# Kernel tuning notes

Measured on AMD Instinct MI355X. Metric: run time of the kernel, lower is better.

## Reference

```python
import math
import jax, jax.numpy as jnp
import numpy as np

NUM_HEADS = 16

def setup_inputs() -> dict:
    key = jax.random.key(0)
    ks = jax.random.split(key, 6)
    B, S, d = 16, 1024, 1024
    scale = 1.0 / math.sqrt(d)
    x = jax.random.normal(ks[0], (B, S, d), dtype=jnp.float32)
    Wq = jax.random.normal(ks[1], (d, d), dtype=jnp.float32) * scale
    Wk = jax.random.normal(ks[2], (d, d), dtype=jnp.float32) * scale
    Wv = jax.random.normal(ks[3], (d, d), dtype=jnp.float32) * scale
    Wo = jax.random.normal(ks[4], (d, d), dtype=jnp.float32) * scale
    z = jnp.zeros((d,), dtype=jnp.float32)
    return {"x": x, "Wq": Wq, "bq": z, "Wk": Wk, "bk": z, "Wv": Wv, "bv": z, "Wo": Wo, "bo": z}

def _split_heads(t, H):
    B, S, d = t.shape
    return t.reshape(B, S, H, d // H).transpose(0, 2, 1, 3)  # [B,H,S,dh]

def reference(x, Wq, bq, Wk, bk, Wv, bv, Wo, bo):
    B, S, d = x.shape
    H = NUM_HEADS
    dh = d // H
    # torch Linear: x @ W.T + b
    Q = _split_heads(x @ Wq.T + bq, H)
    K = _split_heads(x @ Wk.T + bk, H)
    V = _split_heads(x @ Wv.T + bv, H)
    scores = jnp.einsum('bhqd,bhkd->bhqk', Q, K)  # [B,H,S,S]
    causal = jnp.arange(S)[None, :] <= jnp.arange(S)[:, None]  # [S,S] True = allowed
    mask = (1.0 - causal.astype(jnp.float32)) * -100000.0
    # NOTE: original divides (scores + mask) by sqrt(dh), mask included
    attn = jax.nn.softmax((scores + mask) / math.sqrt(dh), axis=-1)
    out = jnp.einsum('bhqk,bhkd->bhqd', attn, V)  # [B,H,S,dh]
    out = out.transpose(0, 2, 1, 3).reshape(B, S, d)
    return out @ Wo.T + bo
```

## Files before the change

### kernel.cpp

```cpp
#include <hip/hip_runtime.h>

#define B_  16
#define S_  1024
#define D_  1024
#define H_  16
#define DH_ 64
#define M_  (B_ * S_)
#define BH_ (B_ * H_)

typedef __attribute__((ext_vector_type(8))) __bf16 bf16x8;
typedef __attribute__((ext_vector_type(4))) float  f32x4;

__device__ __forceinline__ ushort f2bf(float f) {
  unsigned u = __builtin_bit_cast(unsigned, f);
  return (ushort)((u + 0x7FFFu + ((u >> 16) & 1u)) >> 16);
}

__device__ __forceinline__ bf16x8 ld8(const ushort* p) {
  return *(const bf16x8*)p;
}

__device__ __forceinline__ float fast_exp2(float x) {
  return __builtin_amdgcn_exp2f(x);
}

__device__ __forceinline__ void gl_lds16(const void* g, void* s) {
  __builtin_amdgcn_global_load_lds((__attribute__((address_space(1))) void*)g,
                                   (__attribute__((address_space(3))) void*)s,
                                   16, 0, 0);
}

__global__ void cvt4(const float* __restrict__ s, ushort* __restrict__ d, int n4) {
  int i = blockIdx.x * 256 + threadIdx.x;
  if (i < n4) {
    const float4 v = ((const float4*)s)[i];
    ushort4 o;
    o.x = f2bf(v.x); o.y = f2bf(v.y); o.z = f2bf(v.z); o.w = f2bf(v.w);
    ((ushort4*)d)[i] = o;
  }
}

template <int MODE>
__global__ void gemm_bt(const ushort* __restrict__ A, const ushort* __restrict__ W,
                        const float* __restrict__ bias, ushort* __restrict__ outH,
                        float* __restrict__ outF, int M, int N, int K) {
  __shared__ ushort lA[128 * 32];
  __shared__ ushort lB[128 * 32];
  const int w  = threadIdx.x >> 6;
  const int l  = threadIdx.x & 63;
  const int m0 = blockIdx.y * 128, n0 = blockIdx.x * 128;
  const int srow = (w << 4) + (l >> 2);
  const int scol = (l & 3) << 3;
  const int lr = l & 15, qd = l >> 4;
  const int wm = (w >> 1) << 6, wn = (w & 1) << 6;

  const f32x4 z = {0.f, 0.f, 0.f, 0.f};
  f32x4 acc[4][4];
#pragma unroll
  for (int i = 0; i < 4; i++)
#pragma unroll
    for (int j = 0; j < 4; j++) acc[i][j] = z;

  for (int k0 = 0; k0 < K; k0 += 32) {
#pragma unroll
    for (int r = 0; r < 2; r++) {
      const int row = r * 64 + srow;
      gl_lds16(A + (size_t)(m0 + row) * K + k0 + scol, &lA[row * 32 + scol]);
      gl_lds16(W + (size_t)(n0 + row) * K + k0 + scol, &lB[row * 32 + scol]);
    }
    __syncthreads();
    bf16x8 af[4], bf_[4];
#pragma unroll
    for (int t = 0; t < 4; t++) {
      af[t]  = ld8(&lA[(wm + t * 16 + lr) * 32 + qd * 8]);
      bf_[t] = ld8(&lB[(wn + t * 16 + lr) * 32 + qd * 8]);
    }
#pragma unroll
    for (int i = 0; i < 4; i++)
#pragma unroll
      for (int j = 0; j < 4; j++)
        acc[i][j] = __builtin_amdgcn_mfma_f32_16x16x32_bf16(af[i], bf_[j], acc[i][j], 0, 0, 0);
    __syncthreads();
  }

#pragma unroll
  for (int j = 0; j < 4; j++) {
    const int n = n0 + wn + j * 16 + lr;
    const float bv = bias[n];
#pragma unroll
    for (int i = 0; i < 4; i++) {
      const f32x4 v = acc[i][j];
#pragma unroll
      for (int r = 0; r < 4; r++) {
        const int m = m0 + wm + i * 16 + qd * 4 + r;
        const float val = v[r] + bv;
        if (MODE == 2) {
          outF[(size_t)m * N + n] = val;
        } else {
          const int b = m >> 10, s = m & 1023, h = n >> 6, dc = n & 63;
          if (MODE == 0)
            outH[((size_t)(b * H_ + h) * S_ + s) * DH_ + dc] = f2bf(val);
          else
            outH[((size_t)(b * H_ + h) * DH_ + dc) * S_ + s] = f2bf(val);
        }
      }
    }
  }
}

#define PSTR 40
__global__ __launch_bounds__(256) void attn_kernel(
    const ushort* __restrict__ Q, const ushort* __restrict__ K,
    const ushort* __restrict__ Vt, ushort* __restrict__ O) {
  __shared__ ushort lP[4][64 * PSTR];
  const int bh = blockIdx.y;
  const int w = threadIdx.x >> 6, l = threadIdx.x & 63;
  const int lr = l & 15, qd = l >> 4;
  const int q0 = (blockIdx.x * 4 + w) * 64;
  const size_t base = (size_t)bh * (S_ * DH_);
  const ushort* Qb = Q + base;
  const ushort* Kb = K + base;
  const ushort* Vb = Vt + (size_t)bh * (DH_ * S_);
  ushort* myP = &lP[w][0];

  bf16x8 bq[4][2];
#pragma unroll
  for (int qt = 0; qt < 4; qt++)
#pragma unroll
    for (int kc = 0; kc < 2; kc++)
      bq[qt][kc] = ld8(Qb + (size_t)(q0 + qt * 16 + lr) * DH_ + kc * 32 + qd * 8);

  const f32x4 z = {0.f, 0.f, 0.f, 0.f};
  f32x4 acc[4][4];
#pragma unroll
  for (int i = 0; i < 4; i++)
#pragma unroll
    for (int j = 0; j < 4; j++) acc[i][j] = z;
  float li[4] = {0.f, 0.f, 0.f, 0.f};

  const float C = 0.18033688011112042f;

  for (int kb = 0; kb < q0 + 64; kb += 32) {
    bf16x8 ak[2][2];
#pragma unroll
    for (int kt = 0; kt < 2; kt++)
#pragma unroll
      for (int kc = 0; kc < 2; kc++)
        ak[kt][kc] = ld8(Kb + (size_t)(kb + kt * 16 + lr) * DH_ + kc * 32 + qd * 8);
    bf16x8 av[4];
#pragma unroll
    for (int dt = 0; dt < 4; dt++)
      av[dt] = ld8(Vb + (size_t)(dt * 16 + lr) * S_ + kb + qd * 8);

    const bool diag = (kb + 31 >= q0);
#pragma unroll
    for (int kt = 0; kt < 2; kt++) {
      const int keyb = kb + kt * 16 + qd * 4;
#pragma unroll
      for (int qt = 0; qt < 4; qt++) {
        f32x4 s = z;
        s = __builtin_amdgcn_mfma_f32_16x16x32_bf16(ak[kt][0], bq[qt][0], s, 0, 0, 0);
        s = __builtin_amdgcn_mfma_f32_16x16x32_bf16(ak[kt][1], bq[qt][1], s, 0, 0, 0);
        const int qq = q0 + qt * 16 + lr;
        float e0 = s[0] * C, e1 = s[1] * C, e2 = s[2] * C, e3 = s[3] * C;
        if (diag) {
          e0 = (keyb + 0 <= qq) ? e0 : -1e30f;
          e1 = (keyb + 1 <= qq) ? e1 : -1e30f;
          e2 = (keyb + 2 <= qq) ? e2 : -1e30f;
          e3 = (keyb + 3 <= qq) ? e3 : -1e30f;
        }
        const float p0 = fast_exp2(e0), p1 = fast_exp2(e1);
        const float p2 = fast_exp2(e2), p3 = fast_exp2(e3);
        li[qt] += (p0 + p1) + (p2 + p3);
        const uint d0 = __builtin_amdgcn_perm(__builtin_bit_cast(uint, p1),
                                              __builtin_bit_cast(uint, p0), 0x07060302u);
        const uint d1 = __builtin_amdgcn_perm(__builtin_bit_cast(uint, p3),
                                              __builtin_bit_cast(uint, p2), 0x07060302u);
        uint2 pk; pk.x = d0; pk.y = d1;
        *(uint2*)(myP + (qt * 16 + lr) * PSTR + kt * 16 + qd * 4) = pk;
      }
    }
#pragma unroll
    for (int qt = 0; qt < 4; qt++) {
      const bf16x8 bp = ld8(myP + (qt * 16 + lr) * PSTR + qd * 8);
#pragma unroll
      for (int dt = 0; dt < 4; dt++)
        acc[dt][qt] = __builtin_amdgcn_mfma_f32_16x16x32_bf16(av[dt], bp, acc[dt][qt], 0, 0, 0);
    }
  }

  const int b = bh >> 4, h = bh & 15;
#pragma unroll
  for (int qt = 0; qt < 4; qt++) {
    float s = li[qt];
    s += __shfl_xor(s, 16);
    s += __shfl_xor(s, 32);
    const float inv = 1.f / s;
    const int q = q0 + qt * 16 + lr;
    ushort* orow = O + ((size_t)(b * S_ + q) * D_) + h * DH_ + qd * 4;
#pragma unroll
    for (int dt = 0; dt < 4; dt++) {
      const f32x4 v = acc[dt][qt];
      uint2 pk;
      pk.x = (uint)f2bf(v[0] * inv) | ((uint)f2bf(v[1] * inv) << 16);
      pk.y = (uint)f2bf(v[2] * inv) | ((uint)f2bf(v[3] * inv) << 16);
      *(uint2*)(orow + dt * 16) = pk;
    }
  }
}

extern "C" void kernel_launch(void* const* d_in, const int* in_sizes, int n_in,
                              void* d_out, int out_size, void* d_ws, size_t ws_size,
                              hipStream_t stream) {
  const float* x  = (const float*)d_in[0];
  const float* Wq = (const float*)d_in[1];
  const float* bq = (const float*)d_in[2];
  const float* Wk = (const float*)d_in[3];
  const float* bk = (const float*)d_in[4];
  const float* Wv = (const float*)d_in[5];
  const float* bv = (const float*)d_in[6];
  const float* Wo = (const float*)d_in[7];
  const float* bo = (const float*)d_in[8];
  float* out = (float*)d_out;

  char* ws = (char*)d_ws;
  ushort* xb   = (ushort*)(ws);
  ushort* qb   = (ushort*)(ws + 33554432);
  ushort* kb   = (ushort*)(ws + 67108864);
  ushort* vtb  = (ushort*)(ws + 100663296);
  ushort* attn = (ushort*)(ws + 134217728);
  ushort* wqb  = (ushort*)(ws + 167772160);
  ushort* wkb  = (ushort*)(ws + 169869312);
  ushort* wvb  = (ushort*)(ws + 171966464);
  ushort* wob  = (ushort*)(ws + 174063616);

  cvt4<<<16384, 256, 0, stream>>>(x,  xb,  4194304);
  cvt4<<<1024,  256, 0, stream>>>(Wq, wqb, 262144);
  cvt4<<<1024,  256, 0, stream>>>(Wk, wkb, 262144);
  cvt4<<<1024,  256, 0, stream>>>(Wv, wvb, 262144);
  cvt4<<<1024,  256, 0, stream>>>(Wo, wob, 262144);

  dim3 g(D_ / 128, M_ / 128);
  gemm_bt<0><<<g, 256, 0, stream>>>(xb, wqb, bq, qb,  nullptr, M_, D_, D_);
  gemm_bt<0><<<g, 256, 0, stream>>>(xb, wkb, bk, kb,  nullptr, M_, D_, D_);
  gemm_bt<1><<<g, 256, 0, stream>>>(xb, wvb, bv, vtb, nullptr, M_, D_, D_);

  attn_kernel<<<dim3(4, BH_), 256, 0, stream>>>(qb, kb, vtb, attn);

  gemm_bt<2><<<g, 256, 0, stream>>>(attn, wob, bo, nullptr, out, M_, D_, D_);
}
```

Before: 469.0 us.

## Fuse QKV projections into one GEMM and balance causal attention work per wave

Replaces three separate projection GEMM launches with one launch over a concatenated weight matrix, choosing bias and output layout per column block. The attention kernel now has each wave process a pair of query tiles (p and 15-p), so causal work is equal across waves and blocks, with half as many blocks. Fewer blocks lowers parallelism, and the fused GEMM relies on the converted weights being contiguous in the workspace.

```diff
diff --git a/kernel.cpp b/kernel.cpp
--- a/kernel.cpp
+++ b/kernel.cpp
@@ -40,10 +40,10 @@
   }
 }
 
-template <int MODE>
-__global__ void gemm_bt(const ushort* __restrict__ A, const ushort* __restrict__ W,
-                        const float* __restrict__ bias, ushort* __restrict__ outH,
-                        float* __restrict__ outF, int M, int N, int K) {
+__global__ void gemm_qkv(const ushort* __restrict__ A, const ushort* __restrict__ Wqkv,
+                         const float* __restrict__ bqp, const float* __restrict__ bkp,
+                         const float* __restrict__ bvp, ushort* __restrict__ qO,
+                         ushort* __restrict__ kO, ushort* __restrict__ vtO) {
   __shared__ ushort lA[128 * 32];
   __shared__ ushort lB[128 * 32];
   const int w  = threadIdx.x >> 6;
@@ -53,6 +53,76 @@
   const int scol = (l & 3) << 3;
   const int lr = l & 15, qd = l >> 4;
   const int wm = (w >> 1) << 6, wn = (w & 1) << 6;
+  const int K = D_;
+
+  const f32x4 z = {0.f, 0.f, 0.f, 0.f};
+  f32x4 acc[4][4];
+#pragma unroll
+  for (int i = 0; i < 4; i++)
+#pragma unroll
+    for (int j = 0; j < 4; j++) acc[i][j] = z;
+
+  for (int k0 = 0; k0 < K; k0 += 32) {
+#pragma unroll
+    for (int r = 0; r < 2; r++) {
+      const int row = r * 64 + srow;
+      gl_lds16(A    + (size_t)(m0 + row) * K + k0 + scol, &lA[row * 32 + scol]);
+      gl_lds16(Wqkv + (size_t)(n0 + row) * K + k0 + scol, &lB[row * 32 + scol]);
+    }
+    __syncthreads();
+    bf16x8 af[4], bf_[4];
+#pragma unroll
+    for (int t = 0; t < 4; t++) {
+      af[t]  = ld8(&lA[(wm + t * 16 + lr) * 32 + qd * 8]);
+      bf_[t] = ld8(&lB[(wn + t * 16 + lr) * 32 + qd * 8]);
+    }
+#pragma unroll
+    for (int i = 0; i < 4; i++)
+#pragma unroll
+      for (int j = 0; j < 4; j++)
+        acc[i][j] = __builtin_amdgcn_mfma_f32_16x16x32_bf16(af[i], bf_[j], acc[i][j], 0, 0, 0);
+    __syncthreads();
+  }
+
+  const int proj = n0 >> 10;
+  const float* bias = (proj == 0) ? bqp : (proj == 1) ? bkp : bvp;
+  ushort* outH = (proj == 0) ? qO : (proj == 1) ? kO : vtO;
+  const int nb = n0 & 1023;
+
+#pragma unroll
+  for (int j = 0; j < 4; j++) {
+    const int n = nb + wn + j * 16 + lr;
+    const float bv = bias[n];
+    const int h = n >> 6, dc = n & 63;
+#pragma unroll
+    for (int i = 0; i < 4; i++) {
+      const f32x4 v = acc[i][j];
+#pragma unroll
+      for (int r = 0; r < 4; r++) {
+        const int m = m0 + wm + i * 16 + qd * 4 + r;
+        const int b = m >> 10, s = m & 1023;
+        const float val = v[r] + bv;
+        if (proj < 2)
+          outH[((size_t)(b * H_ + h) * S_ + s) * DH_ + dc] = f2bf(val);
+        else
+          outH[((size_t)(b * H_ + h) * DH_ + dc) * S_ + s] = f2bf(val);
+      }
+    }
+  }
+}
+
+__global__ void gemm_out(const ushort* __restrict__ A, const ushort* __restrict__ W,
+                         const float* __restrict__ bias, float* __restrict__ outF) {
+  __shared__ ushort lA[128 * 32];
+  __shared__ ushort lB[128 * 32];
+  const int w  = threadIdx.x >> 6;
+  const int l  = threadIdx.x & 63;
+  const int m0 = blockIdx.y * 128, n0 = blockIdx.x * 128;
+  const int srow = (w << 4) + (l >> 2);
+  const int scol = (l & 3) << 3;
+  const int lr = l & 15, qd = l >> 4;
+  const int wm = (w >> 1) << 6, wn = (w & 1) << 6;
+  const int K = D_, N = D_;
 
   const f32x4 z = {0.f, 0.f, 0.f, 0.f};
   f32x4 acc[4][4];
@@ -93,16 +163,7 @@
 #pragma unroll
       for (int r = 0; r < 4; r++) {
         const int m = m0 + wm + i * 16 + qd * 4 + r;
-        const float val = v[r] + bv;
-        if (MODE == 2) {
-          outF[(size_t)m * N + n] = val;
-        } else {
-          const int b = m >> 10, s = m & 1023, h = n >> 6, dc = n & 63;
-          if (MODE == 0)
-            outH[((size_t)(b * H_ + h) * S_ + s) * DH_ + dc] = f2bf(val);
-          else
-            outH[((size_t)(b * H_ + h) * DH_ + dc) * S_ + s] = f2bf(val);
-        }
+        outF[(size_t)m * N + n] = v[r] + bv;
       }
     }
   }
@@ -116,95 +177,99 @@
   const int bh = blockIdx.y;
   const int w = threadIdx.x >> 6, l = threadIdx.x & 63;
   const int lr = l & 15, qd = l >> 4;
-  const int q0 = (blockIdx.x * 4 + w) * 64;
+  const int p = blockIdx.x * 4 + w;
   const size_t base = (size_t)bh * (S_ * DH_);
   const ushort* Qb = Q + base;
   const ushort* Kb = K + base;
   const ushort* Vb = Vt + (size_t)bh * (DH_ * S_);
   ushort* myP = &lP[w][0];
-
-  bf16x8 bq[4][2];
-#pragma unroll
-  for (int qt = 0; qt < 4; qt++)
-#pragma unroll
-    for (int kc = 0; kc < 2; kc++)
-      bq[qt][kc] = ld8(Qb + (size_t)(q0 + qt * 16 + lr) * DH_ + kc * 32 + qd * 8);
-
+  const int b = bh >> 4, h = bh & 15;
+  const float C = 0.18033688011112042f;
   const f32x4 z = {0.f, 0.f, 0.f, 0.f};
-  f32x4 acc[4][4];
-#pragma unroll
-  for (int i = 0; i < 4; i++)
-#pragma unroll
-    for (int j = 0; j < 4; j++) acc[i][j] = z;
-  float li[4] = {0.f, 0.f, 0.f, 0.f};
-
-  const float C = 0.18033688011112042f;
-
-  for (int kb = 0; kb < q0 + 64; kb += 32) {
-    bf16x8 ak[2][2];
-#pragma unroll
-    for (int kt = 0; kt < 2; kt++)
+
+#pragma unroll 1
+  for (int tt = 0; tt < 2; tt++) {
+    const int q0 = (tt == 0 ? p : 15 - p) * 64;
+
+    bf16x8 bq[4][2];
+#pragma unroll
+    for (int qt = 0; qt < 4; qt++)
 #pragma unroll
       for (int kc = 0; kc < 2; kc++)
-        ak[kt][kc] = ld8(Kb + (size_t)(kb + kt * 16 + lr) * DH_ + kc * 32 + qd * 8);
-    bf16x8 av[4];
-#pragma unroll
-    for (int dt = 0; dt < 4; dt++)
-      av[dt] = ld8(Vb + (size_t)(dt * 16 + lr) * S_ + kb + qd * 8);
-
-    const bool diag = (kb + 31 >= q0);
-#pragma unroll
-    for (int kt = 0; kt < 2; kt++) {
-      const int keyb = kb + kt * 16 + qd * 4;
+        bq[qt][kc] = ld8(Qb + (size_t)(q0 + qt * 16 + lr) * DH_ + kc * 32 + qd * 8);
+
+    f32x4 acc[4][4];
+#pragma unroll
+    for (int i = 0; i < 4; i++)
+#pragma unroll
+      for (int j = 0; j < 4; j++) acc[i][j] = z;
+    float li[4] = {0.f, 0.f, 0.f, 0.f};
+
+    for (int kb = 0; kb < q0 + 64; kb += 32) {
+      bf16x8 ak[2][2];
+#pragma unroll
+      for (int kt = 0; kt < 2; kt++)
+#pragma unroll
+        for (int kc = 0; kc < 2; kc++)
+          ak[kt][kc] = ld8(Kb + (size_t)(kb + kt * 16 + lr) * DH_ + kc * 32 + qd * 8);
+      bf16x8 av[4];
+#pragma unroll
+      for (int dt = 0; dt < 4; dt++)
+        av[dt] = ld8(Vb + (size_t)(dt * 16 + lr) * S_ + kb + qd * 8);
+
+      const bool diag = (kb + 31 >= q0);
+#pragma unroll
+      for (int kt = 0; kt < 2; kt++) {
+        const int keyb = kb + kt * 16 + qd * 4;
+#pragma unroll
+        for (int qt = 0; qt < 4; qt++) {
+          f32x4 s = z;
+          s = __builtin_amdgcn_mfma_f32_16x16x32_bf16(ak[kt][0], bq[qt][0], s, 0, 0, 0);
+          s = __builtin_amdgcn_mfma_f32_16x16x32_bf16(ak[kt][1], bq[qt][1], s, 0, 0, 0);
+          const int qq = q0 + qt * 16 + lr;
+          float e0 = s[0] * C, e1 = s[1] * C, e2 = s[2] * C, e3 = s[3] * C;
+          if (diag) {
+            e0 = (keyb + 0 <= qq) ? e0 : -1e30f;
+            e1 = (keyb + 1 <= qq) ? e1 : -1e30f;
+            e2 = (keyb + 2 <= qq) ? e2 : -1e30f;
+            e3 = (keyb + 3 <= qq) ? e3 : -1e30f;
+          }
+          const float p0 = fast_exp2(e0), p1 = fast_exp2(e1);
+          const float p2 = fast_exp2(e2), p3 = fast_exp2(e3);
+          li[qt] += (p0 + p1) + (p2 + p3);
+          const uint d0 = __builtin_amdgcn_perm(__builtin_bit_cast(uint, p1),
+                                                __builtin_bit_cast(uint, p0), 0x07060302u);
+          const uint d1 = __builtin_amdgcn_perm(__builtin_bit_cast(uint, p3),
+                                                __builtin_bit_cast(uint, p2), 0x07060302u);
+          uint2 pk; pk.x = d0; pk.y = d1;
+          *(uint2*)(myP + (qt * 16 + lr) * PSTR + kt * 16 + qd * 4) = pk;
+        }
+      }
 #pragma unroll
       for (int qt = 0; qt < 4; qt++) {
-        f32x4 s = z;
-        s = __builtin_amdgcn_mfma_f32_16x16x32_bf16(ak[kt][0], bq[qt][0], s, 0, 0, 0);
-        s = __builtin_amdgcn_mfma_f32_16x16x32_bf16(ak[kt][1], bq[qt][1], s, 0, 0, 0);
-        const int qq = q0 + qt * 16 + lr;
-        float e0 = s[0] * C, e1 = s[1] * C, e2 = s[2] * C, e3 = s[3] * C;
-        if (diag) {
-          e0 = (keyb + 0 <= qq) ? e0 : -1e30f;
-          e1 = (keyb + 1 <= qq) ? e1 : -1e30f;
-          e2 = (keyb + 2 <= qq) ? e2 : -1e30f;
-          e3 = (keyb + 3 <= qq) ? e3 : -1e30f;
-        }
-        const float p0 = fast_exp2(e0), p1 = fast_exp2(e1);
-        const float p2 = fast_exp2(e2), p3 = fast_exp2(e3);
-        li[qt] += (p0 + p1) + (p2 + p3);
-        const uint d0 = __builtin_amdgcn_perm(__builtin_bit_cast(uint, p1),
-                                              __builtin_bit_cast(uint, p0), 0x07060302u);
-        const uint d1 = __builtin_amdgcn_perm(__builtin_bit_cast(uint, p3),
-                                              __builtin_bit_cast(uint, p2), 0x07060302u);
-        uint2 pk; pk.x = d0; pk.y = d1;
-        *(uint2*)(myP + (qt * 16 + lr) * PSTR + kt * 16 + qd * 4) = pk;
-      }
-    }
+        const bf16x8 bp = ld8(myP + (qt * 16 + lr) * PSTR + qd * 8);
+#pragma unroll
+        for (int dt = 0; dt < 4; dt++)
+          acc[dt][qt] = __builtin_amdgcn_mfma_f32_16x16x32_bf16(av[dt], bp, acc[dt][qt], 0, 0, 0);
+      }
+    }
+
 #pragma unroll
     for (int qt = 0; qt < 4; qt++) {
-      const bf16x8 bp = ld8(myP + (qt * 16 + lr) * PSTR + qd * 8);
-#pragma unroll
-      for (int dt = 0; dt < 4; dt++)
-        acc[dt][qt] = __builtin_amdgcn_mfma_f32_16x16x32_bf16(av[dt], bp, acc[dt][qt], 0, 0, 0);
-    }
-  }
-
-  const int b = bh >> 4, h = bh & 15;
-#pragma unroll
-  for (int qt = 0; qt < 4; qt++) {
-    float s = li[qt];
-    s += __shfl_xor(s, 16);
-    s += __shfl_xor(s, 32);
-    const float inv = 1.f / s;
-    const int q = q0 + qt * 16 + lr;
-    ushort* orow = O + ((size_t)(b * S_ + q) * D_) + h * DH_ + qd * 4;
-#pragma unroll
-    for (int dt = 0; dt < 4; dt++) {
-      const f32x4 v = acc[dt][qt];
-      uint2 pk;
-      pk.x = (uint)f2bf(v[0] * inv) | ((uint)f2bf(v[1] * inv) << 16);
-      pk.y = (uint)f2bf(v[2] * inv) | ((uint)f2bf(v[3] * inv) << 16);
-      *(uint2*)(orow + dt * 16) = pk;
+      float s = li[qt];
+      s += __shfl_xor(s, 16);
+      s += __shfl_xor(s, 32);
+      const float inv = 1.f / s;
+      const int q = q0 + qt * 16 + lr;
+      ushort* orow = O + ((size_t)(b * S_ + q) * D_) + h * DH_ + qd * 4;
+#pragma unroll
+      for (int dt = 0; dt < 4; dt++) {
+        const f32x4 v = acc[dt][qt];
+        uint2 pk;
+        pk.x = (uint)f2bf(v[0] * inv) | ((uint)f2bf(v[1] * inv) << 16);
+        pk.y = (uint)f2bf(v[2] * inv) | ((uint)f2bf(v[3] * inv) << 16);
+        *(uint2*)(orow + dt * 16) = pk;
+      }
     }
   }
 }
@@ -240,12 +305,9 @@
   cvt4<<<1024,  256, 0, stream>>>(Wv, wvb, 262144);
   cvt4<<<1024,  256, 0, stream>>>(Wo, wob, 262144);
 
-  dim3 g(D_ / 128, M_ / 128);
-  gemm_bt<0><<<g, 256, 0, stream>>>(xb, wqb, bq, qb,  nullptr, M_, D_, D_);
-  gemm_bt<0><<<g, 256, 0, stream>>>(xb, wkb, bk, kb,  nullptr, M_, D_, D_);
-  gemm_bt<1><<<g, 256, 0, stream>>>(xb, wvb, bv, vtb, nullptr, M_, D_, D_);
-
-  attn_kernel<<<dim3(4, BH_), 256, 0, stream>>>(qb, kb, vtb, attn);
-
-  gemm_bt<2><<<g, 256, 0, stream>>>(attn, wob, bo, nullptr, out, M_, D_, D_);
-}
+  gemm_qkv<<<dim3(24, 128), 256, 0, stream>>>(xb, wqb, bq, bk, bv, qb, kb, vtb);
+
+  attn_kernel<<<dim3(2, BH_), 256, 0, stream>>>(qb, kb, vtb, attn);
+
+  gemm_out<<<dim3(8, 128), 256, 0, stream>>>(attn, wob, bo, out);
+}
```

Result: faster. 426.3 us (-9.1%).
